# Kernel optimization log

Measured on AMD Instinct MI355X. Metric: run time of the kernel, lower is better.

## Reference

```python
import jax, jax.numpy as jnp
import numpy as np

NEG = -9e15

def setup_inputs() -> dict:
    key = jax.random.key(0)
    k1, k2, k3, k4 = jax.random.split(key, 4)
    N, Fin, Fout = 8192, 256, 256
    h = jax.random.normal(k1, (N, Fin), dtype=jnp.float32)
    adj = jax.random.randint(k2, (N, N), 0, 2).astype(jnp.float32)
    W = jax.random.normal(k3, (Fin, Fout), dtype=jnp.float32) * (1.414 * np.sqrt(2.0 / (Fin + Fout)))
    a = jax.random.normal(k4, (2 * Fout, 1), dtype=jnp.float32) * (1.414 * np.sqrt(2.0 / (2 * Fout + 1)))
    return {"h": h, "adj": adj, "W": W, "a": a}

def reference(h, adj, W, a):
    Fout = W.shape[1]
    Wh = h @ W                                  # [N, Fout]
    Wh1 = Wh @ a[:Fout, :]                      # [N, 1]
    Wh2 = Wh @ a[Fout:, :]                      # [N, 1]
    e = jax.nn.leaky_relu(Wh1 + Wh2.T, 0.2)     # [N, N]
    mask = (adj > 0).astype(e.dtype)
    e = e * mask + NEG * (1.0 - mask)
    attention = jax.nn.softmax(e, axis=1)       # [N, N]
    h_prime = attention @ Wh                    # [N, Fout]
    return jax.nn.elu(h_prime)
```

## Files before the change

kernel.cpp:

```cpp
#include <hip/hip_runtime.h>
#include <hip/hip_bf16.h>
#include <stdint.h>

typedef __attribute__((ext_vector_type(4))) short short4v;
typedef __attribute__((ext_vector_type(8))) short short8v;
typedef __attribute__((ext_vector_type(4))) float float4v;

#define NN 8192
#define FIN 256
#define FOUT 256

__device__ __forceinline__ short f2bf(float f) {
    unsigned u = __float_as_uint(f);
    unsigned r = u + 0x7fffu + ((u >> 16) & 1u);
    return (short)(r >> 16);
}

__global__ __launch_bounds__(256) void k_wt(const float* __restrict__ W, short* __restrict__ WT) {
    int k = blockIdx.x, n = threadIdx.x;
    WT[n * 256 + k] = f2bf(W[k * 256 + n]);
}

__global__ __launch_bounds__(256) void k_gemm1(const float* __restrict__ h, const short* __restrict__ WT,
                                               float* __restrict__ Wh) {
    __shared__ short sA[64 * 40];
    __shared__ short sB[64 * 40];
    int bm = blockIdx.x;
    int bn = blockIdx.y;
    int t  = threadIdx.x;
    int w = t >> 6, lane = t & 63, quad = lane >> 4, l16 = lane & 15;

    float4v acc[4];
#pragma unroll
    for (int c = 0; c < 4; c++)
#pragma unroll
        for (int j = 0; j < 4; j++) acc[c][j] = 0.f;

    int r  = t >> 2;
    int ko = (t & 3) * 8;

    for (int k0 = 0; k0 < 256; k0 += 32) {
        const float4v* src = (const float4v*)&h[(size_t)(64 * bm + r) * 256 + k0 + ko];
        float4v v0 = src[0], v1 = src[1];
        short8v pk;
        pk[0] = f2bf(v0[0]); pk[1] = f2bf(v0[1]); pk[2] = f2bf(v0[2]); pk[3] = f2bf(v0[3]);
        pk[4] = f2bf(v1[0]); pk[5] = f2bf(v1[1]); pk[6] = f2bf(v1[2]); pk[7] = f2bf(v1[3]);
        *(short8v*)&sA[r * 40 + ko] = pk;
        short8v bv = *(const short8v*)&WT[(size_t)(64 * bn + r) * 256 + k0 + ko];
        *(short8v*)&sB[r * 40 + ko] = bv;
        __syncthreads();

        short8v af = *(const short8v*)&sA[(16 * w + l16) * 40 + quad * 8];
#pragma unroll
        for (int c = 0; c < 4; c++) {
            short8v bf = *(const short8v*)&sB[(16 * c + l16) * 40 + quad * 8];
            acc[c] = __builtin_amdgcn_mfma_f32_16x16x32_bf16(af, bf, acc[c], 0, 0, 0);
        }
        __syncthreads();
    }
#pragma unroll
    for (int c = 0; c < 4; c++)
#pragma unroll
        for (int j = 0; j < 4; j++) {
            int row = 64 * bm + 16 * w + quad * 4 + j;
            int col = 64 * bn + 16 * c + l16;
            Wh[(size_t)row * 256 + col] = acc[c][j];
        }
}

__global__ __launch_bounds__(256) void k_rowstats(const float* __restrict__ Wh, const float* __restrict__ a,
                                                  float* __restrict__ Wh1, float* __restrict__ Wh2,
                                                  unsigned* __restrict__ maxenc) {
    int w = threadIdx.x >> 6, lane = threadIdx.x & 63;
    int row = blockIdx.x * 4 + w;
    float s1 = 0.f, s2 = 0.f;
#pragma unroll
    for (int j = 0; j < 4; j++) {
        int c = lane + 64 * j;
        float v = Wh[(size_t)row * 256 + c];
        s1 += v * a[c];
        s2 += v * a[256 + c];
    }
#pragma unroll
    for (int off = 32; off; off >>= 1) {
        s1 += __shfl_down(s1, off);
        s2 += __shfl_down(s2, off);
    }
    if (lane == 0) {
        Wh1[row] = s1;
        Wh2[row] = s2;
        unsigned u = __float_as_uint(s2);
        unsigned key = (u & 0x80000000u) ? ~u : (u | 0x80000000u);
        atomicMax(maxenc, key);
    }
}

__global__ __launch_bounds__(256) void k_transpose(const float* __restrict__ Wh, short* __restrict__ WhT) {
    __shared__ short sT[64 * 72];
    int bm = blockIdx.x, bn = blockIdx.y;
    int t = threadIdx.x;
#pragma unroll
    for (int i = 0; i < 4; i++) {
        int idx = i * 256 + t;
        int r = idx >> 4, c4 = (idx & 15) * 4;
        float4v v = *(const float4v*)&Wh[(size_t)(64 * bm + r) * 256 + 64 * bn + c4];
#pragma unroll
        for (int j = 0; j < 4; j++) sT[(c4 + j) * 72 + r] = f2bf(v[j]);
    }
    __syncthreads();
    int c = t >> 2, ro = (t & 3) * 16;
#pragma unroll
    for (int hh = 0; hh < 2; hh++) {
        short8v v = *(const short8v*)&sT[c * 72 + ro + 8 * hh];
        *(short8v*)&WhT[(size_t)(64 * bn + c) * 8192 + 64 * bm + ro + 8 * hh] = v;
    }
}

__global__ __launch_bounds__(512, 2) void k_gat(const float* __restrict__ adj, const short* __restrict__ WhT,
                                                const float* __restrict__ Wh1, const float* __restrict__ Wh2,
                                                const unsigned* __restrict__ maxenc,
                                                float* __restrict__ Cacc, float* __restrict__ Lacc,
                                                int Ksub) {
    __shared__ short sB[2][256 * 64];
    __shared__ short sA[64 * 72];
    int bm = blockIdx.x;
    int sidx = blockIdx.y;
    int kb = sidx * Ksub;
    int t = threadIdx.x;
    int lane = t & 63, quad = lane >> 4, l16 = lane & 15;
    int w = t >> 6;
    int mr = (w >> 2) * 32;
    int cg = w & 3;

    unsigned key = maxenc[0];
    unsigned u = (key & 0x80000000u) ? (key & 0x7fffffffu) : ~key;
    float maxw2 = __uint_as_float(u);

    int r  = t >> 3;
    int kc = (t & 7) * 8;
    float wh1r = Wh1[64 * bm + r];
    float sup = wh1r + maxw2;
    float ci = fmaxf(sup, 0.2f * sup);

    const float* adj_row = &adj[(size_t)(64 * bm + r) * 8192 + kb];
    const float* w2base  = &Wh2[kb];

    int nrow = t >> 1;
    int half = t & 1;
    const short* gB = &WhT[(size_t)nrow * 8192 + kb + half * 32];
    int nx = nrow & 7;
    int sbw0 = nrow * 64 + (((half * 4 + 0) ^ nx)) * 8;
    int sbw1 = nrow * 64 + (((half * 4 + 1) ^ nx)) * 8;
    int sbw2 = nrow * 64 + (((half * 4 + 2) ^ nx)) * 8;
    int sbw3 = nrow * 64 + (((half * 4 + 3) ^ nx)) * 8;

    float4v acc[2][4];
#pragma unroll
    for (int rt = 0; rt < 2; rt++)
#pragma unroll
        for (int c = 0; c < 4; c++)
#pragma unroll
            for (int j = 0; j < 4; j++) acc[rt][c][j] = 0.f;
    float lsum = 0.f;

    short8v a0, a1, a2, a3;
    short8v b0, b1, b2, b3;
    float4v av0, av1, w20, w21;
    float4v cv0, cv1, x20, x21;

    av0 = *(const float4v*)&adj_row[kc];
    av1 = *(const float4v*)&adj_row[kc + 4];
    w20 = *(const float4v*)&w2base[kc];
    w21 = *(const float4v*)&w2base[kc + 4];
    a0 = *(const short8v*)&gB[0];
    a1 = *(const short8v*)&gB[8];
    a2 = *(const short8v*)&gB[16];
    a3 = *(const short8v*)&gB[24];
    *(short8v*)&sB[0][sbw0] = a0;
    *(short8v*)&sB[0][sbw1] = a1;
    *(short8v*)&sB[0][sbw2] = a2;
    *(short8v*)&sB[0][sbw3] = a3;
    b0 = *(const short8v*)&gB[64];
    b1 = *(const short8v*)&gB[64 + 8];
    b2 = *(const short8v*)&gB[64 + 16];
    b3 = *(const short8v*)&gB[64 + 24];

#define STAGE(K0, CUR, C0, C1, C2, C3, N0, N1, N2, N3, AV0, AV1, AW0, AW1, NV0, NV1, NW0, NW1)   \
    {                                                                                            \
        int k1 = (K0) + 64, k2 = (K0) + 128;                                                     \
        if (k1 < Ksub) {                                                                         \
            NV0 = *(const float4v*)&adj_row[k1 + kc];                                            \
            NV1 = *(const float4v*)&adj_row[k1 + kc + 4];                                        \
            NW0 = *(const float4v*)&w2base[k1 + kc];                                             \
            NW1 = *(const float4v*)&w2base[k1 + kc + 4];                                         \
        }                                                                                        \
        if (k2 < Ksub) {                                                                         \
            N0 = *(const short8v*)&gB[k2];                                                       \
            N1 = *(const short8v*)&gB[k2 + 8];                                                   \
            N2 = *(const short8v*)&gB[k2 + 16];                                                  \
            N3 = *(const short8v*)&gB[k2 + 24];                                                  \
        }                                                                                        \
        if (k1 < Ksub) {                                                                         \
            *(short8v*)&sB[(CUR) ^ 1][sbw0] = C0;                                                \
            *(short8v*)&sB[(CUR) ^ 1][sbw1] = C1;                                                \
            *(short8v*)&sB[(CUR) ^ 1][sbw2] = C2;                                                \
            *(short8v*)&sB[(CUR) ^ 1][sbw3] = C3;                                                \
        }                                                                                        \
        short8v pk;                                                                              \
        _Pragma("unroll")                                                                        \
        for (int j = 0; j < 4; j++) {                                                            \
            float s = wh1r + AW0[j];                                                             \
            float f = fmaxf(s, 0.2f * s);                                                        \
            float p = __expf(f - ci);                                                            \
            p = (AV0[j] > 0.f) ? p : 0.f;                                                        \
            lsum += p;                                                                           \
            pk[j] = f2bf(p);                                                                     \
        }                                                                                        \
        _Pragma("unroll")                                                                        \
        for (int j = 0; j < 4; j++) {                                                            \
            float s = wh1r + AW1[j];                                                             \
            float f = fmaxf(s, 0.2f * s);                                                        \
            float p = __expf(f - ci);                                                            \
            p = (AV1[j] > 0.f) ? p : 0.f;                                                        \
            lsum += p;                                                                           \
            pk[4 + j] = f2bf(p);                                                                 \
        }                                                                                        \
        *(short8v*)&sA[r * 72 + kc] = pk;                                                        \
        asm volatile("s_waitcnt lgkmcnt(0)" ::: "memory");                                       \
        __builtin_amdgcn_s_barrier();                                                            \
        __builtin_amdgcn_s_setprio(1);                                                           \
        {                                                                                        \
            const short* sBc = &sB[(CUR)][0];                                                    \
            _Pragma("unroll")                                                                    \
            for (int kk = 0; kk < 2; kk++) {                                                     \
                short8v af0 = *(const short8v*)&sA[(mr + l16) * 72 + kk * 32 + quad * 8];        \
                short8v af1 = *(const short8v*)&sA[(mr + 16 + l16) * 72 + kk * 32 + quad * 8];   \
                _Pragma("unroll")                                                                \
                for (int c = 0; c < 4; c++) {                                                    \
                    int n = 64 * cg + 16 * c + l16;                                              \
                    int ch = (kk * 4 + quad) ^ (n & 7);                                          \
                    short8v bf = *(const short8v*)&sBc[n * 64 + ch * 8];                         \
                    acc[0][c] = __builtin_amdgcn_mfma_f32_16x16x32_bf16(af0, bf, acc[0][c], 0, 0, 0); \
                    acc[1][c] = __builtin_amdgcn_mfma_f32_16x16x32_bf16(af1, bf, acc[1][c], 0, 0, 0); \
                }                                                                                \
            }                                                                                    \
        }                                                                                        \
        __builtin_amdgcn_s_setprio(0);                                                           \
        __builtin_amdgcn_s_barrier();                                                            \
    }

    for (int k0 = 0; k0 < Ksub; k0 += 128) {
        STAGE(k0,      0, b0, b1, b2, b3, a0, a1, a2, a3, av0, av1, w20, w21, cv0, cv1, x20, x21)
        STAGE(k0 + 64, 1, a0, a1, a2, a3, b0, b1, b2, b3, cv0, cv1, x20, x21, av0, av1, w20, w21)
    }
#undef STAGE

#pragma unroll
    for (int off = 4; off; off >>= 1) lsum += __shfl_xor(lsum, off, 8);
    if ((t & 7) == 0) atomicAdd(&Lacc[64 * bm + r], lsum);

#pragma unroll
    for (int rt = 0; rt < 2; rt++)
#pragma unroll
        for (int c = 0; c < 4; c++)
#pragma unroll
            for (int j = 0; j < 4; j++) {
                int row = 64 * bm + mr + rt * 16 + quad * 4 + j;
                int col = 64 * cg + 16 * c + l16;
                atomicAdd(&Cacc[(size_t)row * 256 + col], acc[rt][c][j]);
            }
}

__global__ __launch_bounds__(256) void k_final(const float* __restrict__ Cacc, const float* __restrict__ Lacc,
                                               float* __restrict__ out) {
    int idx = blockIdx.x * 256 + threadIdx.x;
    int row = idx >> 6;
    int c4 = (idx & 63) * 4;
    float4v v = *(const float4v*)&Cacc[(size_t)row * 256 + c4];
    float inv = 1.0f / fmaxf(Lacc[row], 1e-30f);
    float4v o;
#pragma unroll
    for (int j = 0; j < 4; j++) {
        float x = v[j] * inv;
        o[j] = (x > 0.f) ? x : (__expf(x) - 1.f);
    }
    *(float4v*)&out[(size_t)row * 256 + c4] = o;
}

extern "C" void kernel_launch(void* const* d_in, const int* in_sizes, int n_in,
                              void* d_out, int out_size, void* d_ws, size_t ws_size,
                              hipStream_t stream) {
    const float* h   = (const float*)d_in[0];
    const float* adj = (const float*)d_in[1];
    const float* W   = (const float*)d_in[2];
    const float* a   = (const float*)d_in[3];
    float* out = (float*)d_out;

    const int S = 4;
    const int Ksub = NN / S;

    char* ws = (char*)d_ws;
    float*    Wh     = (float*)(ws);
    float*    Cacc   = (float*)(ws);
    short*    WhT    = (short*)(ws + 8388608);
    char*     tail   = ws + 12582912;
    short*    WT     = (short*)(tail);
    float*    Wh1    = (float*)(tail + 131072);
    float*    Wh2    = (float*)(tail + 163840);
    float*    Lacc   = (float*)(tail + 196608);
    unsigned* maxenc = (unsigned*)(tail + 229376);

    hipMemsetAsync(maxenc, 0, sizeof(unsigned), stream);

    k_wt<<<256, 256, 0, stream>>>(W, WT);
    k_gemm1<<<dim3(128, 4), 256, 0, stream>>>(h, WT, Wh);
    k_rowstats<<<2048, 256, 0, stream>>>(Wh, a, Wh1, Wh2, maxenc);
    k_transpose<<<dim3(128, 4), 256, 0, stream>>>(Wh, WhT);
    hipMemsetAsync(Cacc, 0, (size_t)NN * 256 * sizeof(float), stream);
    hipMemsetAsync(Lacc, 0, (size_t)NN * sizeof(float), stream);
    k_gat<<<dim3(128, S), 512, 0, stream>>>(adj, WhT, Wh1, Wh2, maxenc, Cacc, Lacc, Ksub);
    k_final<<<2048, 256, 0, stream>>>(Cacc, Lacc, out);
}
```

Baseline: 568.5 us.

## Replace split-K atomics with 32-row full-K tiles and fused softmax/ELU epilogue

The attention kernel no longer splits the neighbour dimension four ways and accumulates partial outputs with atomics. Instead each block owns 32 rows, walks all 8192 columns, and normalises plus applies ELU in-register before writing output directly. This removes the Cacc/Lacc memsets, the atomic traffic and the separate finalisation kernel. The cost is that each block reloads the full WhT matrix for only 32 rows, which doubles B-operand traffic per output row and halves MFMA work per barrier. The grid also shrinks to 256 blocks of long sequential loops.

```diff
diff --git a/kernel.cpp b/kernel.cpp
--- a/kernel.cpp
+++ b/kernel.cpp
@@ -119,59 +119,54 @@
 __global__ __launch_bounds__(512, 2) void k_gat(const float* __restrict__ adj, const short* __restrict__ WhT,
                                                 const float* __restrict__ Wh1, const float* __restrict__ Wh2,
                                                 const unsigned* __restrict__ maxenc,
-                                                float* __restrict__ Cacc, float* __restrict__ Lacc,
-                                                int Ksub) {
+                                                float* __restrict__ out) {
     __shared__ short sB[2][256 * 64];
-    __shared__ short sA[64 * 72];
+    __shared__ short sA[32 * 72];
+    __shared__ float sL[32];
     int bm = blockIdx.x;
-    int sidx = blockIdx.y;
-    int kb = sidx * Ksub;
+    int brow = bm * 32;
     int t = threadIdx.x;
     int lane = t & 63, quad = lane >> 4, l16 = lane & 15;
     int w = t >> 6;
-    int mr = (w >> 2) * 32;
+    int rg = w >> 2;
     int cg = w & 3;
 
     unsigned key = maxenc[0];
     unsigned u = (key & 0x80000000u) ? (key & 0x7fffffffu) : ~key;
     float maxw2 = __uint_as_float(u);
 
-    int r  = t >> 3;
-    int kc = (t & 7) * 8;
-    float wh1r = Wh1[64 * bm + r];
+    int r  = t >> 4;
+    int kc = (t & 15) * 4;
+    float wh1r = Wh1[brow + r];
     float sup = wh1r + maxw2;
     float ci = fmaxf(sup, 0.2f * sup);
 
-    const float* adj_row = &adj[(size_t)(64 * bm + r) * 8192 + kb];
-    const float* w2base  = &Wh2[kb];
+    const float* adj_row = &adj[(size_t)(brow + r) * 8192];
+    const float* w2base  = Wh2;
 
     int nrow = t >> 1;
     int half = t & 1;
-    const short* gB = &WhT[(size_t)nrow * 8192 + kb + half * 32];
+    const short* gB = &WhT[(size_t)nrow * 8192 + half * 32];
     int nx = nrow & 7;
     int sbw0 = nrow * 64 + (((half * 4 + 0) ^ nx)) * 8;
     int sbw1 = nrow * 64 + (((half * 4 + 1) ^ nx)) * 8;
     int sbw2 = nrow * 64 + (((half * 4 + 2) ^ nx)) * 8;
     int sbw3 = nrow * 64 + (((half * 4 + 3) ^ nx)) * 8;
 
-    float4v acc[2][4];
-#pragma unroll
-    for (int rt = 0; rt < 2; rt++)
-#pragma unroll
-        for (int c = 0; c < 4; c++)
-#pragma unroll
-            for (int j = 0; j < 4; j++) acc[rt][c][j] = 0.f;
+    float4v acc[4];
+#pragma unroll
+    for (int c = 0; c < 4; c++)
+#pragma unroll
+        for (int j = 0; j < 4; j++) acc[c][j] = 0.f;
     float lsum = 0.f;
 
     short8v a0, a1, a2, a3;
     short8v b0, b1, b2, b3;
-    float4v av0, av1, w20, w21;
-    float4v cv0, cv1, x20, x21;
-
-    av0 = *(const float4v*)&adj_row[kc];
-    av1 = *(const float4v*)&adj_row[kc + 4];
-    w20 = *(const float4v*)&w2base[kc];
-    w21 = *(const float4v*)&w2base[kc + 4];
+    float4v av, w2v;
+    float4v cv, x2v;
+
+    av  = *(const float4v*)&adj_row[kc];
+    w2v = *(const float4v*)&w2base[kc];
     a0 = *(const short8v*)&gB[0];
     a1 = *(const short8v*)&gB[8];
     a2 = *(const short8v*)&gB[16];
@@ -185,47 +180,36 @@
     b2 = *(const short8v*)&gB[64 + 16];
     b3 = *(const short8v*)&gB[64 + 24];
 
-#define STAGE(K0, CUR, C0, C1, C2, C3, N0, N1, N2, N3, AV0, AV1, AW0, AW1, NV0, NV1, NW0, NW1)   \
+#define STAGE(K0, CUR, C0, C1, C2, C3, N0, N1, N2, N3, AV, W2V, NAV, NW2V)                       \
     {                                                                                            \
         int k1 = (K0) + 64, k2 = (K0) + 128;                                                     \
-        if (k1 < Ksub) {                                                                         \
-            NV0 = *(const float4v*)&adj_row[k1 + kc];                                            \
-            NV1 = *(const float4v*)&adj_row[k1 + kc + 4];                                        \
-            NW0 = *(const float4v*)&w2base[k1 + kc];                                             \
-            NW1 = *(const float4v*)&w2base[k1 + kc + 4];                                         \
-        }                                                                                        \
-        if (k2 < Ksub) {                                                                         \
+        if (k1 < NN) {                                                                           \
+            NAV  = *(const float4v*)&adj_row[k1 + kc];                                           \
+            NW2V = *(const float4v*)&w2base[k1 + kc];                                            \
+        }                                                                                        \
+        if (k2 < NN) {                                                                           \
             N0 = *(const short8v*)&gB[k2];                                                       \
             N1 = *(const short8v*)&gB[k2 + 8];                                                   \
             N2 = *(const short8v*)&gB[k2 + 16];                                                  \
             N3 = *(const short8v*)&gB[k2 + 24];                                                  \
         }                                                                                        \
-        if (k1 < Ksub) {                                                                         \
+        if (k1 < NN) {                                                                           \
             *(short8v*)&sB[(CUR) ^ 1][sbw0] = C0;                                                \
             *(short8v*)&sB[(CUR) ^ 1][sbw1] = C1;                                                \
             *(short8v*)&sB[(CUR) ^ 1][sbw2] = C2;                                                \
             *(short8v*)&sB[(CUR) ^ 1][sbw3] = C3;                                                \
         }                                                                                        \
-        short8v pk;                                                                              \
+        short4v pk;                                                                              \
         _Pragma("unroll")                                                                        \
         for (int j = 0; j < 4; j++) {                                                            \
-            float s = wh1r + AW0[j];                                                             \
+            float s = wh1r + W2V[j];                                                             \
             float f = fmaxf(s, 0.2f * s);                                                        \
             float p = __expf(f - ci);                                                            \
-            p = (AV0[j] > 0.f) ? p : 0.f;                                                        \
+            p = (AV[j] > 0.f) ? p : 0.f;                                                         \
             lsum += p;                                                                           \
             pk[j] = f2bf(p);                                                                     \
         }                                                                                        \
-        _Pragma("unroll")                                                                        \
-        for (int j = 0; j < 4; j++) {                                                            \
-            float s = wh1r + AW1[j];                                                             \
-            float f = fmaxf(s, 0.2f * s);                                                        \
-            float p = __expf(f - ci);                                                            \
-            p = (AV1[j] > 0.f) ? p : 0.f;                                                        \
-            lsum += p;                                                                           \
-            pk[4 + j] = f2bf(p);                                                                 \
-        }                                                                                        \
-        *(short8v*)&sA[r * 72 + kc] = pk;                                                        \
+        *(short4v*)&sA[r * 72 + kc] = pk;                                                        \
         asm volatile("s_waitcnt lgkmcnt(0)" ::: "memory");                                       \
         __builtin_amdgcn_s_barrier();                                                            \
         __builtin_amdgcn_s_setprio(1);                                                           \
@@ -233,15 +217,13 @@
             const short* sBc = &sB[(CUR)][0];                                                    \
             _Pragma("unroll")                                                                    \
             for (int kk = 0; kk < 2; kk++) {                                                     \
-                short8v af0 = *(const short8v*)&sA[(mr + l16) * 72 + kk * 32 + quad * 8];        \
-                short8v af1 = *(const short8v*)&sA[(mr + 16 + l16) * 72 + kk * 32 + quad * 8];   \
+                short8v af = *(const short8v*)&sA[(16 * rg + l16) * 72 + kk * 32 + quad * 8];    \
                 _Pragma("unroll")                                                                \
                 for (int c = 0; c < 4; c++) {                                                    \
                     int n = 64 * cg + 16 * c + l16;                                              \
                     int ch = (kk * 4 + quad) ^ (n & 7);                                          \
                     short8v bf = *(const short8v*)&sBc[n * 64 + ch * 8];                         \
-                    acc[0][c] = __builtin_amdgcn_mfma_f32_16x16x32_bf16(af0, bf, acc[0][c], 0, 0, 0); \
-                    acc[1][c] = __builtin_amdgcn_mfma_f32_16x16x32_bf16(af1, bf, acc[1][c], 0, 0, 0); \
+                    acc[c] = __builtin_amdgcn_mfma_f32_16x16x32_bf16(af, bf, acc[c], 0, 0, 0);   \
                 }                                                                                \
             }                                                                                    \
         }                                                                                        \
@@ -249,42 +231,28 @@
         __builtin_amdgcn_s_barrier();                                                            \
     }
 
-    for (int k0 = 0; k0 < Ksub; k0 += 128) {
-        STAGE(k0,      0, b0, b1, b2, b3, a0, a1, a2, a3, av0, av1, w20, w21, cv0, cv1, x20, x21)
-        STAGE(k0 + 64, 1, a0, a1, a2, a3, b0, b1, b2, b3, cv0, cv1, x20, x21, av0, av1, w20, w21)
+    for (int k0 = 0; k0 < NN; k0 += 128) {
+        STAGE(k0,      0, b0, b1, b2, b3, a0, a1, a2, a3, av, w2v, cv, x2v)
+        STAGE(k0 + 64, 1, a0, a1, a2, a3, b0, b1, b2, b3, cv, x2v, av, w2v)
     }
 #undef STAGE
 
 #pragma unroll
-    for (int off = 4; off; off >>= 1) lsum += __shfl_xor(lsum, off, 8);
-    if ((t & 7) == 0) atomicAdd(&Lacc[64 * bm + r], lsum);
-
-#pragma unroll
-    for (int rt = 0; rt < 2; rt++)
-#pragma unroll
-        for (int c = 0; c < 4; c++)
-#pragma unroll
-            for (int j = 0; j < 4; j++) {
-                int row = 64 * bm + mr + rt * 16 + quad * 4 + j;
-                int col = 64 * cg + 16 * c + l16;
-                atomicAdd(&Cacc[(size_t)row * 256 + col], acc[rt][c][j]);
-            }
-}
-
-__global__ __launch_bounds__(256) void k_final(const float* __restrict__ Cacc, const float* __restrict__ Lacc,
-                                               float* __restrict__ out) {
-    int idx = blockIdx.x * 256 + threadIdx.x;
-    int row = idx >> 6;
-    int c4 = (idx & 63) * 4;
-    float4v v = *(const float4v*)&Cacc[(size_t)row * 256 + c4];
-    float inv = 1.0f / fmaxf(Lacc[row], 1e-30f);
-    float4v o;
+    for (int off = 8; off; off >>= 1) lsum += __shfl_xor(lsum, off, 16);
+    if ((t & 15) == 0) sL[r] = lsum;
+    __syncthreads();
+
 #pragma unroll
     for (int j = 0; j < 4; j++) {
-        float x = v[j] * inv;
-        o[j] = (x > 0.f) ? x : (__expf(x) - 1.f);
-    }
-    *(float4v*)&out[(size_t)row * 256 + c4] = o;
+        int row_l = 16 * rg + quad * 4 + j;
+        float inv = 1.0f / fmaxf(sL[row_l], 1e-30f);
+#pragma unroll
+        for (int c = 0; c < 4; c++) {
+            float x = acc[c][j] * inv;
+            float o = (x > 0.f) ? x : (__expf(x) - 1.f);
+            out[(size_t)(brow + row_l) * 256 + 64 * cg + 16 * c + l16] = o;
+        }
+    }
 }
 
 extern "C" void kernel_launch(void* const* d_in, const int* in_sizes, int n_in,
@@ -296,19 +264,14 @@
     const float* a   = (const float*)d_in[3];
     float* out = (float*)d_out;
 
-    const int S = 4;
-    const int Ksub = NN / S;
-
     char* ws = (char*)d_ws;
     float*    Wh     = (float*)(ws);
-    float*    Cacc   = (float*)(ws);
     short*    WhT    = (short*)(ws + 8388608);
     char*     tail   = ws + 12582912;
     short*    WT     = (short*)(tail);
     float*    Wh1    = (float*)(tail + 131072);
     float*    Wh2    = (float*)(tail + 163840);
-    float*    Lacc   = (float*)(tail + 196608);
-    unsigned* maxenc = (unsigned*)(tail + 229376);
+    unsigned* maxenc = (unsigned*)(tail + 196608);
 
     hipMemsetAsync(maxenc, 0, sizeof(unsigned), stream);
 
@@ -316,8 +279,5 @@
     k_gemm1<<<dim3(128, 4), 256, 0, stream>>>(h, WT, Wh);
     k_rowstats<<<2048, 256, 0, stream>>>(Wh, a, Wh1, Wh2, maxenc);
     k_transpose<<<dim3(128, 4), 256, 0, stream>>>(Wh, WhT);
-    hipMemsetAsync(Cacc, 0, (size_t)NN * 256 * sizeof(float), stream);
-    hipMemsetAsync(Lacc, 0, (size_t)NN * sizeof(float), stream);
-    k_gat<<<dim3(128, S), 512, 0, stream>>>(adj, WhT, Wh1, Wh2, maxenc, Cacc, Lacc, Ksub);
-    k_final<<<2048, 256, 0, stream>>>(Cacc, Lacc, out);
-}
+    k_gat<<<256, 512, 0, stream>>>(adj, WhT, Wh1, Wh2, maxenc, out);
+}
```

After: 616.1 us. 8.4% more time.
